# Performance work log

Hardware: AMD Instinct MI355X
Metric: run time of the kernel (lower is better)

## Reference

```python
import jax, jax.numpy as jnp
import numpy as np

RES = 192      # resolution
RANK = 8       # low-rank
FD = 32        # feature_dim
NFPD = 32      # num_features_per_dim = round(32768**(1/3))
RADIUS = 1.3
NI = 128       # n_intersections
STEP = 0.0352  # step_size
B = 2048       # rays


def setup_inputs():
    key = jax.random.key(0)
    ks = jax.random.split(key, 12)
    ro = jax.random.normal(ks[0], (B, 3), dtype=jnp.float32)
    ro = ro / jnp.linalg.norm(ro, axis=-1, keepdims=True) * 2.5  # origins outside the cube
    rd = -ro + 0.1 * jax.random.normal(ks[1], (B, 3), dtype=jnp.float32)
    rd = rd / jnp.linalg.norm(rd, axis=-1, keepdims=True)        # roughly toward origin
    def nrm(k, shape, std):
        return std * jax.random.normal(k, shape, dtype=jnp.float32)
    return {
        "rays_o": ro, "rays_d": rd,
        "Gxy": nrm(ks[2], (RES, RES, 3, RANK), 0.1),
        "Gxz": nrm(ks[3], (RES, RES, 3, RANK), 0.1),
        "Gyz": nrm(ks[4], (RES, RES, 3, RANK), 0.1),
        "F_grid": nrm(ks[5], (NFPD, NFPD, NFPD, FD), 0.05),
        "sW0": nrm(ks[6], (FD, 128), FD ** -0.5),
        "sW1": nrm(ks[7], (128, 128), 128 ** -0.5),
        "sW2": nrm(ks[8], (128, 16), 128 ** -0.5),
        "cW0": nrm(ks[9], (31, 64), 31 ** -0.5),
        "cW1": nrm(ks[10], (64, 64), 64 ** -0.5),
        "cW2": nrm(ks[11], (64, 3), 64 ** -0.5),
    }


def trilinear(vol, coords):
    # vol: [D,H,W,C]; coords: [N,3] as (x,y,z) in [-1,1]; x indexes W (last spatial dim)
    # matches torch grid_sample(align_corners=True, mode='bilinear', padding_mode='border')
    D, H, W, C = vol.shape
    def prep(c, size):
        idx = jnp.clip((c + 1.0) * 0.5 * (size - 1), 0.0, size - 1.0)  # border clamp
        i0 = jnp.clip(jnp.floor(idx).astype(jnp.int32), 0, size - 2)
        return i0, i0 + 1, idx - i0
    x0, x1, wx = prep(coords[:, 0], W)
    y0, y1, wy = prep(coords[:, 1], H)
    z0, z1, wz = prep(coords[:, 2], D)
    wx = wx[:, None]; wy = wy[:, None]; wz = wz[:, None]
    def g(zi, yi, xi):
        return vol[zi, yi, xi]  # [N,C]
    c00 = g(z0, y0, x0) * (1 - wx) + g(z0, y0, x1) * wx
    c01 = g(z0, y1, x0) * (1 - wx) + g(z0, y1, x1) * wx
    c10 = g(z1, y0, x0) * (1 - wx) + g(z1, y0, x1) * wx
    c11 = g(z1, y1, x0) * (1 - wx) + g(z1, y1, x1) * wx
    c0 = c00 * (1 - wy) + c01 * wy
    c1 = c10 * (1 - wy) + c11 * wy
    return c0 * (1 - wz) + c1 * wz


def sh16(d):
    # tcnn SphericalHarmonics degree 4 on directions (input (d+1)/2 is unmapped back to d internally)
    x, y, z = d[:, 0], d[:, 1], d[:, 2]
    x2, y2, z2 = x * x, y * y, z * z
    return jnp.stack([
        jnp.full_like(x, 0.28209479177387814),
        -0.48860251190291987 * y,
        0.48860251190291987 * z,
        -0.48860251190291987 * x,
        1.0925484305920792 * x * y,
        -1.0925484305920792 * y * z,
        0.94617469575755997 * z2 - 0.31539156525251999,
        -1.0925484305920792 * x * z,
        0.54627421529603959 * (x2 - y2),
        0.59004358992664352 * y * (-3.0 * x2 + y2),
        2.8906114426405538 * x * y * z,
        0.45704579946446572 * y * (1.0 - 5.0 * z2),
        0.3731763325901154 * z * (5.0 * z2 - 3.0),
        0.45704579946446572 * x * (1.0 - 5.0 * z2),
        1.445305721320277 * z * (x2 - y2),
        0.59004358992664352 * x * (-x2 + 3.0 * y2),
    ], axis=-1)


def _forward(rays_o, rays_d, Gxy, Gxz, Gyz, F_grid, sW0, sW1, sW2, cW0, cW1, cW2):
    b = rays_o.shape[0]
    # --- get_intersections: ray/AABB [-R,R]^3, uniform marching ---
    d = jnp.where(jnp.abs(rays_d) < 1e-9, 1e-9, rays_d)
    t1 = (-RADIUS - rays_o) / d
    t2 = (RADIUS - rays_o) / d
    tmin = jnp.max(jnp.minimum(t1, t2), axis=-1)
    tmax = jnp.min(jnp.maximum(t1, t2), axis=-1)
    near = jnp.maximum(tmin, 0.0)
    ts = near[:, None] + jnp.arange(NI + 1, dtype=jnp.float32) * STEP  # intersections [B,NI+1]
    tmid = 0.5 * (ts[:, :-1] + ts[:, 1:])                              # [B,NI]
    pts = rays_o[:, None, :] + tmid[..., None] * rays_d[:, None, :]    # [B,NI,3]
    mask = (jnp.all(jnp.abs(pts) <= RADIUS, axis=-1)
            & (tmid <= tmax[:, None]) & (tmax > tmin)[:, None])        # [B,NI]
    rdn = rays_d / jnp.linalg.norm(rays_d, axis=-1, keepdims=True)
    # coordinate chain of forward + eval_pts nets out to pts/RADIUS in [-1,1]
    p = ((pts / RADIUS + 1.0) * RES / 2.0) * 2.0 / RES - 1.0
    pf = p.reshape(-1, 3)
    # --- densify low-rank tri-plane grid: sum_r Gxy*Gxz*Gyz -> [RES,RES,RES,3] ---
    grid = jnp.zeros((RES, RES, RES, 3), dtype=Gxy.dtype)
    for r in range(RANK):  # fixed small rank; avoids a [RES^3,3,RANK] intermediate
        grid = grid + (Gxy[:, :, None, :, r] * Gxz[:, None, :, :, r] * Gyz[None, :, :, :, r])
    # --- eval_pts: grid_sample -> hash-feature grid_sample -> MLPs ---
    Gvals = trilinear(grid, pf)            # [N,3]
    Fvals = trilinear(F_grid, Gvals)       # [N,FD]
    h = jax.nn.relu(Fvals @ sW0)
    h = jax.nn.relu(h @ sW1)
    out16 = h @ sW2                        # [N,16]
    sigma = out16[:, 0].reshape(b, NI)
    sigma = jax.nn.relu(jnp.where(mask, sigma, 0.0))
    rdn_pts = jnp.broadcast_to(rdn[:, None, :], (b, NI, 3)).reshape(-1, 3)
    ci = jnp.concatenate([sh16(rdn_pts), out16[:, 1:]], axis=-1)  # [N,31]
    c = jax.nn.relu(ci @ cW0)
    c = jax.nn.relu(c @ cW1)
    color = (c @ cW2).reshape(b, NI, 3)
    color = jnp.where(mask[..., None], color, 0.0)
    # --- sigma2alpha + shrgb2rgb (white background) ---
    dists = ts[:, 1:] - ts[:, :-1]         # |rdn| == 1
    alpha = 1.0 - jnp.exp(-sigma * dists)
    T = jnp.cumprod(1.0 - alpha + 1e-10, axis=-1)
    T = jnp.concatenate([jnp.ones_like(T[:, :1]), T[:, :-1]], axis=-1)  # exclusive
    w = alpha * T                          # abs_light [B,NI]
    rgb = jax.nn.sigmoid(color)
    acc = jnp.sum(w, axis=-1)
    return jnp.sum(w[..., None] * rgb, axis=1) + (1.0 - acc)[..., None]  # [B,3]


def reference(rays_o, rays_d, Gxy, Gxz, Gyz, F_grid, sW0, sW1, sW2, cW0, cW1, cW2):
    return _forward(rays_o, rays_d, Gxy, Gxz, Gyz, F_grid, sW0, sW1, sW2, cW0, cW1, cW2)
```

## Files before the change

kernel.cpp:

```cpp
#include <hip/hip_runtime.h>
#include <math.h>

#define RES 192
#define RANK 8
#define NI 128
#define LW 136

typedef __attribute__((ext_vector_type(8))) short short8;
typedef __attribute__((ext_vector_type(4))) float floatx4;

#define OFF_SW0 0
#define OFF_SW1 4096
#define OFF_SW2 20480
#define OFF_CW0 22528
#define OFF_CW1 24576
#define OFF_CW2 28672
#define PACK_TOTAL 29696

#define TRI_CELLS (RES*RES)
#define TRI_TOTAL (3*TRI_CELLS*24)
#define FG_TOTAL  (32*32*32*32)

__device__ __forceinline__ short f2bf(float x){
    unsigned u = __float_as_uint(x);
    unsigned r = (u + 0x7FFFu + ((u >> 16) & 1u)) >> 16;
    return (short)r;
}
__device__ __forceinline__ float bf2f(short s){
    return __uint_as_float(((unsigned)(unsigned short)s) << 16);
}

__device__ __forceinline__ void prep_idx(float c, int size, int& i0, float& f){
    float idx = (c + 1.0f)*0.5f*(float)(size-1);
    idx = fminf(fmaxf(idx, 0.0f), (float)(size-1));
    int ii = (int)idx;
    if (ii > size-2) ii = size-2;
    i0 = ii;
    f = idx - (float)ii;
}

__device__ __forceinline__ float wred64(float v){
    #pragma unroll
    for (int o=32;o>0;o>>=1) v += __shfl_down(v, o, 64);
    return v;
}

__global__ void pack_all(const float* __restrict__ sW0, const float* __restrict__ sW1,
                         const float* __restrict__ sW2, const float* __restrict__ cW0,
                         const float* __restrict__ cW1, const float* __restrict__ cW2,
                         short* __restrict__ dst){
    int e = blockIdx.x*256 + threadIdx.x;
    if (e >= PACK_TOTAL) return;
    const float* src; int K, N, ksteps, base;
    if      (e < OFF_SW1){ src=sW0; K=32;  N=128; ksteps=1; base=OFF_SW0; }
    else if (e < OFF_SW2){ src=sW1; K=128; N=128; ksteps=4; base=OFF_SW1; }
    else if (e < OFF_CW0){ src=sW2; K=128; N=16;  ksteps=4; base=OFF_SW2; }
    else if (e < OFF_CW1){ src=cW0; K=31;  N=64;  ksteps=1; base=OFF_CW0; }
    else if (e < OFF_CW2){ src=cW1; K=64;  N=64;  ksteps=2; base=OFF_CW1; }
    else                 { src=cW2; K=64;  N=3;   ksteps=2; base=OFF_CW2; }
    int i = e - base;
    int j = i & 7, lane = (i>>3)&63, t = i>>9;
    int ks = t % ksteps, nt = t / ksteps;
    int k = ks*32 + (lane>>4)*8 + j;
    int n = nt*16 + (lane&15);
    float v = (k < K && n < N) ? src[k*N + n] : 0.0f;
    dst[e] = f2bf(v);
}

__global__ void conv_tri(const float* __restrict__ Gxy, const float* __restrict__ Gxz,
                         const float* __restrict__ Gyz, short* __restrict__ dst){
    int e = blockIdx.x*256 + threadIdx.x;
    if (e >= TRI_TOTAL) return;
    int p    = e / (TRI_CELLS*24);
    int rem  = e - p*(TRI_CELLS*24);
    int cell = rem / 24;
    int c    = rem - cell*24;
    const float* src = (p==0) ? Gxy : (p==1) ? Gxz : Gyz;
    dst[((size_t)(p*TRI_CELLS + cell))*32 + c] = f2bf(src[(size_t)cell*24 + c]);
}

__global__ void conv_fg(const float* __restrict__ F_grid, short* __restrict__ dst){
    int e = blockIdx.x*256 + threadIdx.x;
    if (e >= FG_TOTAL) return;
    dst[e] = f2bf(F_grid[e]);
}

__global__ void __launch_bounds__(256) interp2(
    const float* __restrict__ rays_o, const float* __restrict__ rays_d,
    const short* __restrict__ Gp, const short* __restrict__ Fg,
    short* __restrict__ FvOut)
{
    const int tid = threadIdx.x;
    const int ray = blockIdx.x;
    const int s   = tid >> 1;
    const int h   = tid & 1;

    const float ox = rays_o[ray*3+0], oy = rays_o[ray*3+1], oz = rays_o[ray*3+2];
    const float dx = rays_d[ray*3+0], dy = rays_d[ray*3+1], dz = rays_d[ray*3+2];

    float sdx = (fabsf(dx) < 1e-9f) ? 1e-9f : dx;
    float sdy = (fabsf(dy) < 1e-9f) ? 1e-9f : dy;
    float sdz = (fabsf(dz) < 1e-9f) ? 1e-9f : dz;
    float t1x = (-1.3f - ox)/sdx, t2x = (1.3f - ox)/sdx;
    float t1y = (-1.3f - oy)/sdy, t2y = (1.3f - oy)/sdy;
    float t1z = (-1.3f - oz)/sdz, t2z = (1.3f - oz)/sdz;
    float tmin = fmaxf(fminf(t1x,t2x), fmaxf(fminf(t1y,t2y), fminf(t1z,t2z)));
    float tmax = fminf(fmaxf(t1x,t2x), fminf(fmaxf(t1y,t2y), fmaxf(t1z,t2z)));
    float nearv = fmaxf(tmin, 0.0f);

    float ts0 = nearv + (float)s     * 0.0352f;
    float ts1 = nearv + (float)(s+1) * 0.0352f;
    float tmid = 0.5f*(ts0+ts1);
    float px = ox + tmid*dx, py = oy + tmid*dy, pz = oz + tmid*dz;
    bool mask = (fabsf(px)<=1.3f) && (fabsf(py)<=1.3f) && (fabsf(pz)<=1.3f)
              && (tmid<=tmax) && (tmax>tmin);

    short8 o0 = {0,0,0,0,0,0,0,0};
    short8 o1 = {0,0,0,0,0,0,0,0};

    if (mask){
        float p0 = (px/1.3f + 1.0f)*192.0f/2.0f*2.0f/192.0f - 1.0f;
        float p1 = (py/1.3f + 1.0f)*192.0f/2.0f*2.0f/192.0f - 1.0f;
        float p2 = (pz/1.3f + 1.0f)*192.0f/2.0f*2.0f/192.0f - 1.0f;

        int x0, y0, z0; float fx, fy, fz;
        prep_idx(p0, RES, x0, fx);
        prep_idx(p1, RES, y0, fy);
        prep_idx(p2, RES, z0, fz);

        const int zi = z0 + h;
        const float wzc = h ? fz : (1.0f - fz);

        short8 XY[2][3], XZ[2][3], YZ[2][2][3];
        {
            const short8* pxy0 = (const short8*)(Gp + ((size_t)(zi*RES + y0  ))*32);
            const short8* pxy1 = (const short8*)(Gp + ((size_t)(zi*RES + y0+1))*32);
            const short8* pxz0 = (const short8*)(Gp + ((size_t)(TRI_CELLS + zi*RES + x0  ))*32);
            const short8* pxz1 = (const short8*)(Gp + ((size_t)(TRI_CELLS + zi*RES + x0+1))*32);
            const short8* pyz00 = (const short8*)(Gp + ((size_t)(2*TRI_CELLS + (y0  )*RES + x0  ))*32);
            const short8* pyz01 = (const short8*)(Gp + ((size_t)(2*TRI_CELLS + (y0  )*RES + x0+1))*32);
            const short8* pyz10 = (const short8*)(Gp + ((size_t)(2*TRI_CELLS + (y0+1)*RES + x0  ))*32);
            const short8* pyz11 = (const short8*)(Gp + ((size_t)(2*TRI_CELLS + (y0+1)*RES + x0+1))*32);
            #pragma unroll
            for (int q=0;q<3;q++){
                XY[0][q]=pxy0[q]; XY[1][q]=pxy1[q];
                XZ[0][q]=pxz0[q]; XZ[1][q]=pxz1[q];
                YZ[0][0][q]=pyz00[q]; YZ[0][1][q]=pyz01[q];
                YZ[1][0][q]=pyz10[q]; YZ[1][1][q]=pyz11[q];
            }
        }

        float gv0=0.f, gv1=0.f, gv2=0.f;
        #pragma unroll
        for (int yc=0; yc<2; yc++){
            const float wy = yc ? fy : (1.0f - fy);
            #pragma unroll
            for (int xc=0; xc<2; xc++){
                const float wx = xc ? fx : (1.0f - fx);
                const float w = wzc*wy*wx;
                float s0=0.f, s1=0.f, s2=0.f;
                #pragma unroll
                for (int r=0;r<8;r++){
                    s0 = fmaf(bf2f(XY[yc][0][r])*bf2f(XZ[xc][0][r]), bf2f(YZ[yc][xc][0][r]), s0);
                    s1 = fmaf(bf2f(XY[yc][1][r])*bf2f(XZ[xc][1][r]), bf2f(YZ[yc][xc][1][r]), s1);
                    s2 = fmaf(bf2f(XY[yc][2][r])*bf2f(XZ[xc][2][r]), bf2f(YZ[yc][xc][2][r]), s2);
                }
                gv0 = fmaf(w, s0, gv0);
                gv1 = fmaf(w, s1, gv1);
                gv2 = fmaf(w, s2, gv2);
            }
        }
        gv0 += __shfl_xor(gv0, 1, 64);
        gv1 += __shfl_xor(gv1, 1, 64);
        gv2 += __shfl_xor(gv2, 1, 64);

        int a0,b0,c0; float fa,fb,fc;
        prep_idx(gv2, 32, a0, fa);
        prep_idx(gv1, 32, b0, fb);
        prep_idx(gv0, 32, c0, fc);
        float Fv[16];
        #pragma unroll
        for (int k=0;k<16;k++) Fv[k]=0.f;
        #pragma unroll
        for (int zc=0; zc<2; zc++){
            const int zi2 = a0+zc; const float wz2 = zc ? fa : 1.f-fa;
            #pragma unroll
            for (int yc=0; yc<2; yc++){
                const int yi2 = b0+yc; const float wy2 = yc ? fb : 1.f-fb;
                #pragma unroll
                for (int xc=0; xc<2; xc++){
                    const int xi2 = c0+xc; const float wx2 = xc ? fc : 1.f-fc;
                    const float w = wz2*wy2*wx2;
                    const short8* pf = (const short8*)(Fg + ((size_t)((zi2*32+yi2)*32+xi2))*32 + h*16);
                    short8 v0 = pf[0], v1 = pf[1];
                    #pragma unroll
                    for (int j=0;j<8;j++){
                        Fv[j]   = fmaf(w, bf2f(v0[j]), Fv[j]);
                        Fv[8+j] = fmaf(w, bf2f(v1[j]), Fv[8+j]);
                    }
                }
            }
        }
        #pragma unroll
        for (int j=0;j<8;j++){ o0[j] = f2bf(Fv[j]); o1[j] = f2bf(Fv[8+j]); }
    }

    short* dstp = FvOut + (((size_t)ray*128 + s)*32 + h*16);
    *(short8*)dstp       = o0;
    *(short8*)(dstp + 8) = o1;
}

__launch_bounds__(256, 2)
__global__ void nerf_mlp(
    const float* __restrict__ rays_o, const float* __restrict__ rays_d,
    const short* __restrict__ Wp, const short* __restrict__ Fv,
    float* __restrict__ out)
{
    __shared__ short buf[128*LW];
    __shared__ float sigmaArr[128];
    __shared__ float rgbArr[128*3];
    __shared__ float wtot[2];
    __shared__ float partial[8];

    const int tid  = threadIdx.x;
    const int lane = tid & 63;
    const int wv   = tid >> 6;
    const int ray  = blockIdx.x;

    const float ox = rays_o[ray*3+0], oy = rays_o[ray*3+1], oz = rays_o[ray*3+2];
    const float dx = rays_d[ray*3+0], dy = rays_d[ray*3+1], dz = rays_d[ray*3+2];

    float sdx = (fabsf(dx) < 1e-9f) ? 1e-9f : dx;
    float sdy = (fabsf(dy) < 1e-9f) ? 1e-9f : dy;
    float sdz = (fabsf(dz) < 1e-9f) ? 1e-9f : dz;
    float t1x = (-1.3f - ox)/sdx, t2x = (1.3f - ox)/sdx;
    float t1y = (-1.3f - oy)/sdy, t2y = (1.3f - oy)/sdy;
    float t1z = (-1.3f - oz)/sdz, t2z = (1.3f - oz)/sdz;
    float tmin = fmaxf(fminf(t1x,t2x), fmaxf(fminf(t1y,t2y), fminf(t1z,t2z)));
    float tmax = fminf(fmaxf(t1x,t2x), fminf(fmaxf(t1y,t2y), fmaxf(t1z,t2z)));
    float nearv = fmaxf(tmin, 0.0f);

    const int rowbase = wv*32;
    const int col  = lane & 15;
    const int quad = lane >> 4;
    const int ar0  = rowbase + col;
    const int ar1  = ar0 + 16;

    {
        const short8* FvG = (const short8*)(Fv + (size_t)ray*128*32);
        short8 a0 = FvG[ar0*4 + quad];
        short8 a1 = FvG[ar1*4 + quad];
        const short8* W = (const short8*)(Wp + OFF_SW0);
        #pragma unroll
        for (int nt=0; nt<8; nt++){
            short8 b = W[nt*64 + lane];
            floatx4 c0v = {0.f,0.f,0.f,0.f}, c1v = {0.f,0.f,0.f,0.f};
            c0v = __builtin_amdgcn_mfma_f32_16x16x32_bf16(a0, b, c0v, 0,0,0);
            c1v = __builtin_amdgcn_mfma_f32_16x16x32_bf16(a1, b, c1v, 0,0,0);
            #pragma unroll
            for (int r=0;r<4;r++){
                int row0 = rowbase + quad*4 + r;
                buf[row0*LW      + nt*16 + col] = f2bf(fmaxf(c0v[r],0.f));
                buf[(row0+16)*LW + nt*16 + col] = f2bf(fmaxf(c1v[r],0.f));
            }
        }
    }

    {
        short8 A0[4], A1[4];
        #pragma unroll
        for (int ks=0;ks<4;ks++){
            A0[ks] = *(const short8*)&buf[ar0*LW + ks*32 + quad*8];
            A1[ks] = *(const short8*)&buf[ar1*LW + ks*32 + quad*8];
        }
        const short8* W = (const short8*)(Wp + OFF_SW1);
        #pragma unroll
        for (int nt=0; nt<8; nt++){
            floatx4 c0v = {0.f,0.f,0.f,0.f}, c1v = {0.f,0.f,0.f,0.f};
            #pragma unroll
            for (int ks=0;ks<4;ks++){
                short8 b = W[(nt*4+ks)*64 + lane];
                c0v = __builtin_amdgcn_mfma_f32_16x16x32_bf16(A0[ks], b, c0v, 0,0,0);
                c1v = __builtin_amdgcn_mfma_f32_16x16x32_bf16(A1[ks], b, c1v, 0,0,0);
            }
            #pragma unroll
            for (int r=0;r<4;r++){
                int row0 = rowbase + quad*4 + r;
                buf[row0*LW      + nt*16 + col] = f2bf(fmaxf(c0v[r],0.f));
                buf[(row0+16)*LW + nt*16 + col] = f2bf(fmaxf(c1v[r],0.f));
            }
        }
    }

    {
        short8 A0[4], A1[4];
        #pragma unroll
        for (int ks=0;ks<4;ks++){
            A0[ks] = *(const short8*)&buf[ar0*LW + ks*32 + quad*8];
            A1[ks] = *(const short8*)&buf[ar1*LW + ks*32 + quad*8];
        }
        const short8* W = (const short8*)(Wp + OFF_SW2);
        floatx4 c0v = {0.f,0.f,0.f,0.f}, c1v = {0.f,0.f,0.f,0.f};
        #pragma unroll
        for (int ks=0;ks<4;ks++){
            short8 b = W[ks*64 + lane];
            c0v = __builtin_amdgcn_mfma_f32_16x16x32_bf16(A0[ks], b, c0v, 0,0,0);
            c1v = __builtin_amdgcn_mfma_f32_16x16x32_bf16(A1[ks], b, c1v, 0,0,0);
        }
        #pragma unroll
        for (int r=0;r<4;r++){
            int row0 = rowbase + quad*4 + r;
            if (col == 0){
                sigmaArr[row0]    = c0v[r];
                sigmaArr[row0+16] = c1v[r];
            } else {
                buf[row0*LW      + 15 + col] = f2bf(c0v[r]);
                buf[(row0+16)*LW + 15 + col] = f2bf(c1v[r]);
            }
        }
        const float dn = sqrtf(dx*dx+dy*dy+dz*dz);
        const float X = dx/dn, Y = dy/dn, Z = dz/dn;
        const float X2=X*X, Y2=Y*Y, Z2=Z*Z;
        float sh[16];
        sh[0]= 0.28209479177387814f;
        sh[1]=-0.48860251190291987f*Y;
        sh[2]= 0.48860251190291987f*Z;
        sh[3]=-0.48860251190291987f*X;
        sh[4]= 1.0925484305920792f*X*Y;
        sh[5]=-1.0925484305920792f*Y*Z;
        sh[6]= 0.94617469575756f*Z2 - 0.31539156525252f;
        sh[7]=-1.0925484305920792f*X*Z;
        sh[8]= 0.5462742152960396f*(X2-Y2);
        sh[9]= 0.5900435899266435f*Y*(-3.0f*X2+Y2);
        sh[10]=2.890611442640554f*X*Y*Z;
        sh[11]=0.4570457994644657f*Y*(1.0f-5.0f*Z2);
        sh[12]=0.3731763325901154f*Z*(5.0f*Z2-3.0f);
        sh[13]=0.4570457994644657f*X*(1.0f-5.0f*Z2);
        sh[14]=1.445305721320277f*Z*(X2-Y2);
        sh[15]=0.5900435899266435f*X*(-X2+3.0f*Y2);
        if (lane < 32){
            int row = rowbase + lane;
            #pragma unroll
            for (int k=0;k<16;k++) buf[row*LW + k] = f2bf(sh[k]);
        }
    }

    {
        short8 a0 = *(const short8*)&buf[ar0*LW + quad*8];
        short8 a1 = *(const short8*)&buf[ar1*LW + quad*8];
        const short8* W = (const short8*)(Wp + OFF_CW0);
        #pragma unroll
        for (int nt=0; nt<4; nt++){
            short8 b = W[nt*64 + lane];
            floatx4 c0v = {0.f,0.f,0.f,0.f}, c1v = {0.f,0.f,0.f,0.f};
            c0v = __builtin_amdgcn_mfma_f32_16x16x32_bf16(a0, b, c0v, 0,0,0);
            c1v = __builtin_amdgcn_mfma_f32_16x16x32_bf16(a1, b, c1v, 0,0,0);
            #pragma unroll
            for (int r=0;r<4;r++){
                int row0 = rowbase + quad*4 + r;
                buf[row0*LW      + nt*16 + col] = f2bf(fmaxf(c0v[r],0.f));
                buf[(row0+16)*LW + nt*16 + col] = f2bf(fmaxf(c1v[r],0.f));
            }
        }
    }

    {
        short8 A0[2], A1[2];
        #pragma unroll
        for (int ks=0;ks<2;ks++){
            A0[ks] = *(const short8*)&buf[ar0*LW + ks*32 + quad*8];
            A1[ks] = *(const short8*)&buf[ar1*LW + ks*32 + quad*8];
        }
        const short8* W = (const short8*)(Wp + OFF_CW1);
        #pragma unroll
        for (int nt=0; nt<4; nt++){
            floatx4 c0v = {0.f,0.f,0.f,0.f}, c1v = {0.f,0.f,0.f,0.f};
            #pragma unroll
            for (int ks=0;ks<2;ks++){
                short8 b = W[(nt*2+ks)*64 + lane];
                c0v = __builtin_amdgcn_mfma_f32_16x16x32_bf16(A0[ks], b, c0v, 0,0,0);
                c1v = __builtin_amdgcn_mfma_f32_16x16x32_bf16(A1[ks], b, c1v, 0,0,0);
            }
            #pragma unroll
            for (int r=0;r<4;r++){
                int row0 = rowbase + quad*4 + r;
                buf[row0*LW      + nt*16 + col] = f2bf(fmaxf(c0v[r],0.f));
                buf[(row0+16)*LW + nt*16 + col] = f2bf(fmaxf(c1v[r],0.f));
            }
        }
    }

    {
        short8 A0[2], A1[2];
        #pragma unroll
        for (int ks=0;ks<2;ks++){
            A0[ks] = *(const short8*)&buf[ar0*LW + ks*32 + quad*8];
            A1[ks] = *(const short8*)&buf[ar1*LW + ks*32 + quad*8];
        }
        const short8* W = (const short8*)(Wp + OFF_CW2);
        floatx4 c0v = {0.f,0.f,0.f,0.f}, c1v = {0.f,0.f,0.f,0.f};
        #pragma unroll
        for (int ks=0;ks<2;ks++){
            short8 b = W[ks*64 + lane];
            c0v = __builtin_amdgcn_mfma_f32_16x16x32_bf16(A0[ks], b, c0v, 0,0,0);
            c1v = __builtin_amdgcn_mfma_f32_16x16x32_bf16(A1[ks], b, c1v, 0,0,0);
        }
        if (col < 3){
            #pragma unroll
            for (int r=0;r<4;r++){
                int row0 = rowbase + quad*4 + r;
                rgbArr[row0*3 + col]      = c0v[r];
                rgbArr[(row0+16)*3 + col] = c1v[r];
            }
        }
    }
    __syncthreads();

    float alpha = 0.f, rr = 0.f, rg = 0.f, rb = 0.f;
    if (tid < 128){
        float ts0 = nearv + (float)tid     * 0.0352f;
        float ts1 = nearv + (float)(tid+1) * 0.0352f;
        float tmid = 0.5f*(ts0+ts1);
        float dist = ts1 - ts0;
        float px = ox + tmid*dx, py = oy + tmid*dy, pz = oz + tmid*dz;
        bool mask = (fabsf(px)<=1.3f) && (fabsf(py)<=1.3f) && (fabsf(pz)<=1.3f)
                  && (tmid<=tmax) && (tmax>tmin);
        float sg = mask ? fmaxf(sigmaArr[tid], 0.f) : 0.f;
        alpha = 1.0f - expf(-sg*dist);
        if (mask){
            rr = 1.0f/(1.0f+expf(-rgbArr[tid*3+0]));
            rg = 1.0f/(1.0f+expf(-rgbArr[tid*3+1]));
            rb = 1.0f/(1.0f+expf(-rgbArr[tid*3+2]));
        }
    }
    float p = 1.0f - alpha + 1e-10f;
    #pragma unroll
    for (int off=1; off<64; off<<=1){
        float u = __shfl_up(p, off, 64);
        if (lane >= off) p *= u;
    }
    if (tid < 128 && lane == 63) wtot[wv] = p;
    float excl = __shfl_up(p, 1, 64);
    if (lane == 0) excl = 1.0f;
    __syncthreads();
    if (tid < 128){
        float T = excl;
        if (wv == 1) T *= wtot[0];
        float w = alpha * T;
        float v0 = wred64(w*rr);
        float v1 = wred64(w*rg);
        float v2 = wred64(w*rb);
        float v3 = wred64(w);
        if (lane == 0){
            partial[wv*4+0]=v0; partial[wv*4+1]=v1; partial[wv*4+2]=v2; partial[wv*4+3]=v3;
        }
    }
    __syncthreads();
    if (tid == 0){
        float acc = partial[3] + partial[7];
        float bg  = 1.0f - acc;
        out[ray*3+0] = partial[0] + partial[4] + bg;
        out[ray*3+1] = partial[1] + partial[5] + bg;
        out[ray*3+2] = partial[2] + partial[6] + bg;
    }
}

extern "C" void kernel_launch(void* const* d_in, const int* in_sizes, int n_in,
                              void* d_out, int out_size, void* d_ws, size_t ws_size,
                              hipStream_t stream){
    const float* rays_o = (const float*)d_in[0];
    const float* rays_d = (const float*)d_in[1];
    const float* Gxy    = (const float*)d_in[2];
    const float* Gxz    = (const float*)d_in[3];
    const float* Gyz    = (const float*)d_in[4];
    const float* F_grid = (const float*)d_in[5];
    const float* sW0    = (const float*)d_in[6];
    const float* sW1    = (const float*)d_in[7];
    const float* sW2    = (const float*)d_in[8];
    const float* cW0    = (const float*)d_in[9];
    const float* cW1    = (const float*)d_in[10];
    const float* cW2    = (const float*)d_in[11];

    short* Wp   = (short*)d_ws;
    short* FvWS = Wp   + PACK_TOTAL;
    short* Gp   = FvWS + (size_t)2048*128*32;
    short* Fg   = Gp   + (size_t)3*TRI_CELLS*32;

    pack_all<<<(PACK_TOTAL+255)/256, 256, 0, stream>>>(sW0,sW1,sW2,cW0,cW1,cW2,Wp);
    conv_tri<<<(TRI_TOTAL+255)/256, 256, 0, stream>>>(Gxy, Gxz, Gyz, Gp);
    conv_fg<<<(FG_TOTAL+255)/256, 256, 0, stream>>>(F_grid, Fg);
    interp2<<<2048, 256, 0, stream>>>(rays_o, rays_d, Gp, Fg, FvWS);
    nerf_mlp<<<2048, 256, 0, stream>>>(rays_o, rays_d, Wp, FvWS, (float*)d_out);
}
```

Baseline: 149.0 us.

## Fuse prep kernels, skip masked MLP warps, pack LDS stores, raise occupancy

```diff
diff --git a/kernel.cpp b/kernel.cpp
--- a/kernel.cpp
+++ b/kernel.cpp
@@ -20,6 +20,7 @@
 #define TRI_CELLS (RES*RES)
 #define TRI_TOTAL (3*TRI_CELLS*24)
 #define FG_TOTAL  (32*32*32*32)
+#define PREP_TOTAL (PACK_TOTAL + TRI_TOTAL + FG_TOTAL)
 
 __device__ __forceinline__ short f2bf(float x){
     unsigned u = __float_as_uint(x);
@@ -45,44 +46,51 @@
     return v;
 }
 
-__global__ void pack_all(const float* __restrict__ sW0, const float* __restrict__ sW1,
-                         const float* __restrict__ sW2, const float* __restrict__ cW0,
-                         const float* __restrict__ cW1, const float* __restrict__ cW2,
-                         short* __restrict__ dst){
+__device__ __forceinline__ void st_pair(short* dst_even, float v, int lane){
+    int bf = (int)(unsigned short)f2bf(v);
+    int nb = __builtin_amdgcn_mov_dpp(bf, 0xB1, 0xF, 0xF, true);
+    int pk = (bf & 0xffff) | (nb << 16);
+    if (!(lane & 1)) *(int*)dst_even = pk;
+}
+
+__global__ void __launch_bounds__(256) prep_all(
+    const float* __restrict__ sW0, const float* __restrict__ sW1,
+    const float* __restrict__ sW2, const float* __restrict__ cW0,
+    const float* __restrict__ cW1, const float* __restrict__ cW2,
+    const float* __restrict__ Gxy, const float* __restrict__ Gxz,
+    const float* __restrict__ Gyz, const float* __restrict__ F_grid,
+    short* __restrict__ Wp, short* __restrict__ Gp, short* __restrict__ Fg)
+{
     int e = blockIdx.x*256 + threadIdx.x;
-    if (e >= PACK_TOTAL) return;
-    const float* src; int K, N, ksteps, base;
-    if      (e < OFF_SW1){ src=sW0; K=32;  N=128; ksteps=1; base=OFF_SW0; }
-    else if (e < OFF_SW2){ src=sW1; K=128; N=128; ksteps=4; base=OFF_SW1; }
-    else if (e < OFF_CW0){ src=sW2; K=128; N=16;  ksteps=4; base=OFF_SW2; }
-    else if (e < OFF_CW1){ src=cW0; K=31;  N=64;  ksteps=1; base=OFF_CW0; }
-    else if (e < OFF_CW2){ src=cW1; K=64;  N=64;  ksteps=2; base=OFF_CW1; }
-    else                 { src=cW2; K=64;  N=3;   ksteps=2; base=OFF_CW2; }
-    int i = e - base;
-    int j = i & 7, lane = (i>>3)&63, t = i>>9;
-    int ks = t % ksteps, nt = t / ksteps;
-    int k = ks*32 + (lane>>4)*8 + j;
-    int n = nt*16 + (lane&15);
-    float v = (k < K && n < N) ? src[k*N + n] : 0.0f;
-    dst[e] = f2bf(v);
-}
-
-__global__ void conv_tri(const float* __restrict__ Gxy, const float* __restrict__ Gxz,
-                         const float* __restrict__ Gyz, short* __restrict__ dst){
-    int e = blockIdx.x*256 + threadIdx.x;
-    if (e >= TRI_TOTAL) return;
-    int p    = e / (TRI_CELLS*24);
-    int rem  = e - p*(TRI_CELLS*24);
-    int cell = rem / 24;
-    int c    = rem - cell*24;
-    const float* src = (p==0) ? Gxy : (p==1) ? Gxz : Gyz;
-    dst[((size_t)(p*TRI_CELLS + cell))*32 + c] = f2bf(src[(size_t)cell*24 + c]);
-}
-
-__global__ void conv_fg(const float* __restrict__ F_grid, short* __restrict__ dst){
-    int e = blockIdx.x*256 + threadIdx.x;
-    if (e >= FG_TOTAL) return;
-    dst[e] = f2bf(F_grid[e]);
+    if (e < PACK_TOTAL){
+        const float* src; int K, N, ksteps, base;
+        if      (e < OFF_SW1){ src=sW0; K=32;  N=128; ksteps=1; base=OFF_SW0; }
+        else if (e < OFF_SW2){ src=sW1; K=128; N=128; ksteps=4; base=OFF_SW1; }
+        else if (e < OFF_CW0){ src=sW2; K=128; N=16;  ksteps=4; base=OFF_SW2; }
+        else if (e < OFF_CW1){ src=cW0; K=31;  N=64;  ksteps=1; base=OFF_CW0; }
+        else if (e < OFF_CW2){ src=cW1; K=64;  N=64;  ksteps=2; base=OFF_CW1; }
+        else                 { src=cW2; K=64;  N=3;   ksteps=2; base=OFF_CW2; }
+        int i = e - base;
+        int j = i & 7, lane = (i>>3)&63, t = i>>9;
+        int ks = t % ksteps, nt = t / ksteps;
+        int k = ks*32 + (lane>>4)*8 + j;
+        int n = nt*16 + (lane&15);
+        float v = (k < K && n < N) ? src[k*N + n] : 0.0f;
+        Wp[e] = f2bf(v);
+        return;
+    }
+    int e2 = e - PACK_TOTAL;
+    if (e2 < TRI_TOTAL){
+        int p    = e2 / (TRI_CELLS*24);
+        int rem  = e2 - p*(TRI_CELLS*24);
+        int cell = rem / 24;
+        int c    = rem - cell*24;
+        const float* src = (p==0) ? Gxy : (p==1) ? Gxz : Gyz;
+        Gp[((size_t)(p*TRI_CELLS + cell))*32 + c] = f2bf(src[(size_t)cell*24 + c]);
+        return;
+    }
+    int e3 = e2 - TRI_TOTAL;
+    Fg[e3] = f2bf(F_grid[e3]);
 }
 
 __global__ void __launch_bounds__(256) interp2(
@@ -210,7 +218,7 @@
     *(short8*)(dstp + 8) = o1;
 }
 
-__launch_bounds__(256, 2)
+__launch_bounds__(256, 4)
 __global__ void nerf_mlp(
     const float* __restrict__ rays_o, const float* __restrict__ rays_d,
     const short* __restrict__ Wp, const short* __restrict__ Fv,
@@ -245,6 +253,18 @@
     const int quad = lane >> 4;
     const int ar0  = rowbase + col;
     const int ar1  = ar0 + 16;
+    const int colp = col & ~1;
+
+    {
+        int sid = rowbase + (lane & 31);
+        float w_ts0 = nearv + (float)sid     * 0.0352f;
+        float w_ts1 = nearv + (float)(sid+1) * 0.0352f;
+        float w_tm  = 0.5f*(w_ts0+w_ts1);
+        float wpx = ox + w_tm*dx, wpy = oy + w_tm*dy, wpz = oz + w_tm*dz;
+        bool m = (fabsf(wpx)<=1.3f) && (fabsf(wpy)<=1.3f) && (fabsf(wpz)<=1.3f)
+               && (w_tm<=tmax) && (tmax>tmin);
+        if (__ballot(m) == 0ULL) goto composite;
+    }
 
     {
         const short8* FvG = (const short8*)(Fv + (size_t)ray*128*32);
@@ -260,8 +280,8 @@
             #pragma unroll
             for (int r=0;r<4;r++){
                 int row0 = rowbase + quad*4 + r;
-                buf[row0*LW      + nt*16 + col] = f2bf(fmaxf(c0v[r],0.f));
-                buf[(row0+16)*LW + nt*16 + col] = f2bf(fmaxf(c1v[r],0.f));
+                st_pair(&buf[row0*LW      + nt*16 + colp], fmaxf(c0v[r],0.f), lane);
+                st_pair(&buf[(row0+16)*LW + nt*16 + colp], fmaxf(c1v[r],0.f), lane);
             }
         }
     }
@@ -286,8 +306,8 @@
             #pragma unroll
             for (int r=0;r<4;r++){
                 int row0 = rowbase + quad*4 + r;
-                buf[row0*LW      + nt*16 + col] = f2bf(fmaxf(c0v[r],0.f));
-                buf[(row0+16)*LW + nt*16 + col] = f2bf(fmaxf(c1v[r],0.f));
+                st_pair(&buf[row0*LW      + nt*16 + colp], fmaxf(c0v[r],0.f), lane);
+                st_pair(&buf[(row0+16)*LW + nt*16 + colp], fmaxf(c1v[r],0.f), lane);
             }
         }
     }
@@ -358,8 +378,8 @@
             #pragma unroll
             for (int r=0;r<4;r++){
                 int row0 = rowbase + quad*4 + r;
-                buf[row0*LW      + nt*16 + col] = f2bf(fmaxf(c0v[r],0.f));
-                buf[(row0+16)*LW + nt*16 + col] = f2bf(fmaxf(c1v[r],0.f));
+                st_pair(&buf[row0*LW      + nt*16 + colp], fmaxf(c0v[r],0.f), lane);
+                st_pair(&buf[(row0+16)*LW + nt*16 + colp], fmaxf(c1v[r],0.f), lane);
             }
         }
     }
@@ -384,8 +404,8 @@
             #pragma unroll
             for (int r=0;r<4;r++){
                 int row0 = rowbase + quad*4 + r;
-                buf[row0*LW      + nt*16 + col] = f2bf(fmaxf(c0v[r],0.f));
-                buf[(row0+16)*LW + nt*16 + col] = f2bf(fmaxf(c1v[r],0.f));
+                st_pair(&buf[row0*LW      + nt*16 + colp], fmaxf(c0v[r],0.f), lane);
+                st_pair(&buf[(row0+16)*LW + nt*16 + colp], fmaxf(c1v[r],0.f), lane);
             }
         }
     }
@@ -414,54 +434,58 @@
             }
         }
     }
+
+composite:
     __syncthreads();
 
-    float alpha = 0.f, rr = 0.f, rg = 0.f, rb = 0.f;
-    if (tid < 128){
-        float ts0 = nearv + (float)tid     * 0.0352f;
-        float ts1 = nearv + (float)(tid+1) * 0.0352f;
-        float tmid = 0.5f*(ts0+ts1);
-        float dist = ts1 - ts0;
-        float px = ox + tmid*dx, py = oy + tmid*dy, pz = oz + tmid*dz;
-        bool mask = (fabsf(px)<=1.3f) && (fabsf(py)<=1.3f) && (fabsf(pz)<=1.3f)
-                  && (tmid<=tmax) && (tmax>tmin);
-        float sg = mask ? fmaxf(sigmaArr[tid], 0.f) : 0.f;
-        alpha = 1.0f - expf(-sg*dist);
-        if (mask){
-            rr = 1.0f/(1.0f+expf(-rgbArr[tid*3+0]));
-            rg = 1.0f/(1.0f+expf(-rgbArr[tid*3+1]));
-            rb = 1.0f/(1.0f+expf(-rgbArr[tid*3+2]));
-        }
-    }
-    float p = 1.0f - alpha + 1e-10f;
-    #pragma unroll
-    for (int off=1; off<64; off<<=1){
-        float u = __shfl_up(p, off, 64);
-        if (lane >= off) p *= u;
-    }
-    if (tid < 128 && lane == 63) wtot[wv] = p;
-    float excl = __shfl_up(p, 1, 64);
-    if (lane == 0) excl = 1.0f;
-    __syncthreads();
-    if (tid < 128){
-        float T = excl;
-        if (wv == 1) T *= wtot[0];
-        float w = alpha * T;
-        float v0 = wred64(w*rr);
-        float v1 = wred64(w*rg);
-        float v2 = wred64(w*rb);
-        float v3 = wred64(w);
-        if (lane == 0){
-            partial[wv*4+0]=v0; partial[wv*4+1]=v1; partial[wv*4+2]=v2; partial[wv*4+3]=v3;
-        }
-    }
-    __syncthreads();
-    if (tid == 0){
-        float acc = partial[3] + partial[7];
-        float bg  = 1.0f - acc;
-        out[ray*3+0] = partial[0] + partial[4] + bg;
-        out[ray*3+1] = partial[1] + partial[5] + bg;
-        out[ray*3+2] = partial[2] + partial[6] + bg;
+    {
+        float alpha = 0.f, rr = 0.f, rg = 0.f, rb = 0.f;
+        if (tid < 128){
+            float ts0 = nearv + (float)tid     * 0.0352f;
+            float ts1 = nearv + (float)(tid+1) * 0.0352f;
+            float tmid = 0.5f*(ts0+ts1);
+            float dist = ts1 - ts0;
+            float px = ox + tmid*dx, py = oy + tmid*dy, pz = oz + tmid*dz;
+            bool mask = (fabsf(px)<=1.3f) && (fabsf(py)<=1.3f) && (fabsf(pz)<=1.3f)
+                      && (tmid<=tmax) && (tmax>tmin);
+            float sg = mask ? fmaxf(sigmaArr[tid], 0.f) : 0.f;
+            alpha = 1.0f - expf(-sg*dist);
+            if (mask){
+                rr = 1.0f/(1.0f+expf(-rgbArr[tid*3+0]));
+                rg = 1.0f/(1.0f+expf(-rgbArr[tid*3+1]));
+                rb = 1.0f/(1.0f+expf(-rgbArr[tid*3+2]));
+            }
+        }
+        float p = 1.0f - alpha + 1e-10f;
+        #pragma unroll
+        for (int off=1; off<64; off<<=1){
+            float u = __shfl_up(p, off, 64);
+            if (lane >= off) p *= u;
+        }
+        if (tid < 128 && lane == 63) wtot[wv] = p;
+        float excl = __shfl_up(p, 1, 64);
+        if (lane == 0) excl = 1.0f;
+        __syncthreads();
+        if (tid < 128){
+            float T = excl;
+            if (wv == 1) T *= wtot[0];
+            float w = alpha * T;
+            float v0 = wred64(w*rr);
+            float v1 = wred64(w*rg);
+            float v2 = wred64(w*rb);
+            float v3 = wred64(w);
+            if (lane == 0){
+                partial[wv*4+0]=v0; partial[wv*4+1]=v1; partial[wv*4+2]=v2; partial[wv*4+3]=v3;
+            }
+        }
+        __syncthreads();
+        if (tid == 0){
+            float acc = partial[3] + partial[7];
+            float bg  = 1.0f - acc;
+            out[ray*3+0] = partial[0] + partial[4] + bg;
+            out[ray*3+1] = partial[1] + partial[5] + bg;
+            out[ray*3+2] = partial[2] + partial[6] + bg;
+        }
     }
 }
 
@@ -486,9 +510,8 @@
     short* Gp   = FvWS + (size_t)2048*128*32;
     short* Fg   = Gp   + (size_t)3*TRI_CELLS*32;
 
-    pack_all<<<(PACK_TOTAL+255)/256, 256, 0, stream>>>(sW0,sW1,sW2,cW0,cW1,cW2,Wp);
-    conv_tri<<<(TRI_TOTAL+255)/256, 256, 0, stream>>>(Gxy, Gxz, Gyz, Gp);
-    conv_fg<<<(FG_TOTAL+255)/256, 256, 0, stream>>>(F_grid, Fg);
+    prep_all<<<PREP_TOTAL/256, 256, 0, stream>>>(sW0,sW1,sW2,cW0,cW1,cW2,
+                                                 Gxy,Gxz,Gyz,F_grid, Wp,Gp,Fg);
     interp2<<<2048, 256, 0, stream>>>(rays_o, rays_d, Gp, Fg, FvWS);
     nerf_mlp<<<2048, 256, 0, stream>>>(rays_o, rays_d, Wp, FvWS, (float*)d_out);
 }
```

Result: slower. 155.8 us (+4.6%).
